# Performance work log

Measured on AMD Instinct MI355X. Metric: run time of the kernel, lower is better.

Reference implementation:

```python
import jax, jax.numpy as jnp
import numpy as np

V, E, H2, T_LEN, B, NTAG = 50257, 512, 1024, 512, 64, 7
H = H2 // 2  # per-direction hidden
START, STOP = 5, 6


def _lstm_dir(x, h0, c0, w_ih, w_hh, b_ih, b_hh, reverse=False):
    # x: [B, T, E]; returns hidden states [B, T, H]
    def step(carry, x_t):
        h, c = carry
        g = x_t @ w_ih.T + b_ih + h @ w_hh.T + b_hh  # [B, 4H]
        i, f, gg, o = jnp.split(g, 4, axis=-1)       # PyTorch gate order i,f,g,o
        c = jax.nn.sigmoid(f) * c + jax.nn.sigmoid(i) * jnp.tanh(gg)
        h = jax.nn.sigmoid(o) * jnp.tanh(c)
        return (h, c), h
    xs = jnp.swapaxes(x, 0, 1)  # [T, B, E]
    _, hs = jax.lax.scan(step, (h0, c0), xs, reverse=reverse)
    return jnp.swapaxes(hs, 0, 1)


def _viterbi(logits, transitions):
    def step(prev, logit_t):  # prev: [B, NTAG]
        v = prev[:, :, None] + transitions[None, :, :]  # [B, prev, next]
        new = logit_t + jnp.max(v, axis=1)
        bp = jnp.argmax(v, axis=1)
        return new, bp
    first = logits[:, 0]
    rest = jnp.swapaxes(logits[:, 1:], 0, 1)  # [T-1, B, NTAG]
    last, bps = jax.lax.scan(step, first, rest)
    scores = jnp.max(last, axis=-1)            # [B]
    last_tag = jnp.argmax(last, axis=-1)       # [B]

    def back(tag, bp_t):  # bp_t: [B, NTAG]
        prev = jnp.take_along_axis(bp_t, tag[:, None], axis=1)[:, 0]
        return prev, prev
    _, earlier = jax.lax.scan(back, last_tag, bps, reverse=True)  # [T-1, B], tags 0..T-2
    paths = jnp.concatenate([jnp.swapaxes(earlier, 0, 1), last_tag[:, None]], axis=1)  # [B, T]
    return scores, paths


def setup_inputs() -> dict:
    key = jax.random.key(0)
    ks = jax.random.split(key, 16)
    s = 1.0 / np.sqrt(H)
    inp = {
        "sentences": jax.random.randint(ks[0], (B, T_LEN), 0, V),
        "emb": jax.random.normal(ks[1], (V, E), jnp.float32),
        "w_ih_f": jax.random.uniform(ks[2], (4 * H, E), jnp.float32, -s, s),
        "w_hh_f": jax.random.uniform(ks[3], (4 * H, H), jnp.float32, -s, s),
        "b_ih_f": jax.random.uniform(ks[4], (4 * H,), jnp.float32, -s, s),
        "b_hh_f": jax.random.uniform(ks[5], (4 * H,), jnp.float32, -s, s),
        "w_ih_b": jax.random.uniform(ks[6], (4 * H, E), jnp.float32, -s, s),
        "w_hh_b": jax.random.uniform(ks[7], (4 * H, H), jnp.float32, -s, s),
        "b_ih_b": jax.random.uniform(ks[8], (4 * H,), jnp.float32, -s, s),
        "b_hh_b": jax.random.uniform(ks[9], (4 * H,), jnp.float32, -s, s),
        "w_out": jax.random.normal(ks[10], (NTAG, H2), jnp.float32) * 0.02,
        "b_out": jnp.zeros((NTAG,), jnp.float32),
        "h0": jax.random.normal(ks[12], (2, B, H), jnp.float32),
        "c0": jax.random.normal(ks[13], (2, B, H), jnp.float32),
    }
    trans = jax.random.normal(ks[14], (NTAG, NTAG), jnp.float32)
    trans = trans.at[START, :].set(-100.0).at[:, STOP].set(-100.0)
    inp["transitions"] = trans
    return inp


def reference(sentences, emb, w_ih_f, w_hh_f, b_ih_f, b_hh_f,
              w_ih_b, w_hh_b, b_ih_b, b_hh_b, w_out, b_out, h0, c0, transitions):
    x = emb[sentences]  # [B, T, E]
    out_f = _lstm_dir(x, h0[0], c0[0], w_ih_f, w_hh_f, b_ih_f, b_hh_f, reverse=False)
    out_b = _lstm_dir(x, h0[1], c0[1], w_ih_b, w_hh_b, b_ih_b, b_hh_b, reverse=True)
    lstm_out = jnp.concatenate([out_f, out_b], axis=-1)  # [B, T, 2H]
    logits = lstm_out @ w_out.T + b_out                  # [B, T, NTAG]
    scores, paths = _viterbi(logits, transitions)
    return scores, paths
```

## Files before the change

kernel.cpp:

```cpp
#include <hip/hip_runtime.h>
#include <cstdint>
#include <cstddef>

#define NTAG 7

typedef unsigned int u32;
typedef unsigned long long u64;
using bf16x8 = __attribute__((ext_vector_type(8))) short;
using f32x4  = __attribute__((ext_vector_type(4))) float;

#define MFMA(A,B,C) __builtin_amdgcn_mfma_f32_16x16x32_bf16((A),(B),(C),0,0,0)

union abf { u64 q[2]; ushort e[8]; bf16x8 v; };

__device__ __forceinline__ u32 rtn_bf16(float f) {
    u32 b = __float_as_uint(f);
    return (b + 0x7fffu + ((b >> 16) & 1u)) >> 16;
}

__global__ __launch_bounds__(256) void prep_w_kernel(
    const float* __restrict__ wif, const float* __restrict__ whf,
    const float* __restrict__ wib, const float* __restrict__ whb,
    ushort* __restrict__ planes)
{
    int f = blockIdx.x * 256 + threadIdx.x;
    int mat = f >> 17;
    int i8 = (f & 0x1FFFF) << 3;
    const float* src = (mat == 0) ? wif : (mat == 1) ? whf : (mat == 2) ? wib : whb;
    float4 v0 = *(const float4*)(src + i8);
    float4 v1 = *(const float4*)(src + i8 + 4);
    ushort o[8];
    const float* pv = (const float*)&v0;
#pragma unroll
    for (int j = 0; j < 4; ++j) o[j] = (ushort)rtn_bf16(pv[j]);
    pv = (const float*)&v1;
#pragma unroll
    for (int j = 0; j < 4; ++j) o[4 + j] = (ushort)rtn_bf16(pv[j]);
    ushort* dst = planes + ((size_t)mat << 20) + i8;
    *(ushort4*)dst = make_ushort4(o[0], o[1], o[2], o[3]);
    *(ushort4*)(dst + 4) = make_ushort4(o[4], o[5], o[6], o[7]);
}

__global__ __launch_bounds__(256) void prep_x_kernel(
    const int* __restrict__ sent, const float* __restrict__ emb,
    ushort* __restrict__ xb)
{
    long f = (long)blockIdx.x * 256 + threadIdx.x;
    long e8 = f << 3;
    int bt = (int)(e8 >> 9);
    int e  = (int)(e8 & 511);
    int tok = sent[bt];
    const float* src = emb + (size_t)tok * 512 + e;
    float4 v0 = *(const float4*)(src);
    float4 v1 = *(const float4*)(src + 4);
    ushort o[8];
    const float* pv = (const float*)&v0;
#pragma unroll
    for (int j = 0; j < 4; ++j) o[j] = (ushort)rtn_bf16(pv[j]);
    pv = (const float*)&v1;
#pragma unroll
    for (int j = 0; j < 4; ++j) o[4 + j] = (ushort)rtn_bf16(pv[j]);
    ushort* dst = xb + e8;
    *(ushort4*)dst = make_ushort4(o[0], o[1], o[2], o[3]);
    *(ushort4*)(dst + 4) = make_ushort4(o[4], o[5], o[6], o[7]);
}

__global__ __launch_bounds__(256, 1) void lstm_mfma_kernel(
    const int* __restrict__ sent, const float* __restrict__ emb,
    const ushort* __restrict__ planes, const ushort* __restrict__ xb,
    const float* __restrict__ bif, const float* __restrict__ bhf,
    const float* __restrict__ bib, const float* __restrict__ bhb,
    const float* __restrict__ wout,
    const float* __restrict__ h0, const float* __restrict__ c0,
    ushort* __restrict__ hglob,
    float* __restrict__ logits,
    int* __restrict__ flags)
{
    __shared__ __align__(16) ushort hstage[16 * 512];
    __shared__ float sums_s[4 * 16 * 33];
    __shared__ float hv_s[16 * 33];
    __shared__ float bias_s[4 * 32];
    __shared__ float wout_s[7 * 33];
    __shared__ float lbuf[8 * 112];

    const int tid = threadIdx.x;
    const int w   = tid >> 6;
    const int L   = tid & 63;
    const int ln  = L & 15;
    const int lk  = L >> 4;
    const int g   = blockIdx.x & 7;
    const int slot= blockIdx.x >> 3;
    const int d   = g & 1;
    const int bq  = g >> 1;
    const int B0  = bq << 4;
    const int u0  = slot << 5;

    const ushort* wip = planes + ((size_t)(d ? 2 : 0) << 20);
    const ushort* whp = planes + ((size_t)(d ? 3 : 1) << 20);

    bf16x8 Bh[2][16];
#pragma unroll
    for (int h = 0; h < 2; ++h) {
        const size_t row = (size_t)(w * 512 + u0 + h * 16 + ln);
#pragma unroll
        for (int kb = 0; kb < 16; ++kb)
            Bh[h][kb] = *(const bf16x8*)(whp + row * 512 + kb * 32 + lk * 8);
    }
    if (tid < 128) {
        int gg = tid >> 5, uu = tid & 31;
        int grow = gg * 512 + u0 + uu;
        bias_s[tid] = d ? (bib[grow] + bhb[grow]) : (bif[grow] + bhf[grow]);
    }
    if (tid < 224) {
        int tg = tid >> 5, uu = tid & 31;
        wout_s[tg * 33 + uu] = wout[(size_t)tg * 1024 + d * 512 + u0 + uu];
    }
    const int cb = tid >> 4, uh = tid & 15;
    float cst[2];
    {
        const float* cr = c0 + ((size_t)(d * 64) + B0 + cb) * 512 + u0 + uh * 2;
        cst[0] = cr[0]; cst[1] = cr[1];
    }
    __syncthreads();

    const int gb = B0 + ln;
    f32x4 xacc0, xacc1;

    auto x_phase = [&](int tnext) {
        f32x4 a0a = {0,0,0,0}, a0b = {0,0,0,0}, a1a = {0,0,0,0}, a1b = {0,0,0,0};
        const size_t row0 = (size_t)(w * 512 + u0 + ln);
        const size_t row1 = row0 + 16;
#pragma unroll
        for (int kb = 0; kb < 16; ++kb) {
            bf16x8 A;
            if (xb) {
                A = *(const bf16x8*)(xb + ((size_t)gb * 512 + tnext) * 512 + kb * 32 + lk * 8);
            } else {
                int tok = sent[gb * 512 + tnext];
                const float* xr = emb + (size_t)tok * 512 + kb * 32 + lk * 8;
                float4 f0 = *(const float4*)(xr);
                float4 f1 = *(const float4*)(xr + 4);
                abf t;
                const float* pv = (const float*)&f0;
#pragma unroll
                for (int j = 0; j < 4; ++j) t.e[j] = (ushort)rtn_bf16(pv[j]);
                pv = (const float*)&f1;
#pragma unroll
                for (int j = 0; j < 4; ++j) t.e[4 + j] = (ushort)rtn_bf16(pv[j]);
                A = t.v;
            }
            bf16x8 Bx0 = *(const bf16x8*)(wip + row0 * 512 + kb * 32 + lk * 8);
            bf16x8 Bx1 = *(const bf16x8*)(wip + row1 * 512 + kb * 32 + lk * 8);
            if (kb & 1) { a0b = MFMA(A, Bx0, a0b); a1b = MFMA(A, Bx1, a1b); }
            else        { a0a = MFMA(A, Bx0, a0a); a1a = MFMA(A, Bx1, a1a); }
        }
        xacc0 = a0a + a0b;
        xacc1 = a1a + a1b;
    };

    x_phase(d ? 511 : 0);

    const char* hsb = (const char*)hstage;
    const int hx = (ln & 7) << 4;

    for (int s = 0; s < 512; ++s) {
        const int t = d ? (511 - s) : s;

        if (s > 0 && w == 0) {
            const int* fp = flags + (g << 4) + (L & 15);
            while (true) {
                int v = __hip_atomic_load(fp, __ATOMIC_RELAXED, __HIP_MEMORY_SCOPE_AGENT);
                if (__all(v >= s)) break;
                __builtin_amdgcn_s_sleep(1);
            }
        }
        __syncthreads();

        f32x4 f0a = xacc0, f0b = {0,0,0,0}, f1a = xacc1, f1b = {0,0,0,0};
        if (s == 0) {
            const float* hr = h0 + ((size_t)(d * 64) + gb) * 512;
#pragma unroll
            for (int kb = 0; kb < 16; ++kb) {
                float4 q0 = *(const float4*)(hr + kb * 32 + lk * 8);
                float4 q1 = *(const float4*)(hr + kb * 32 + lk * 8 + 4);
                abf A;
                const float* pv = (const float*)&q0;
#pragma unroll
                for (int j = 0; j < 4; ++j) A.e[j] = (ushort)rtn_bf16(pv[j]);
                pv = (const float*)&q1;
#pragma unroll
                for (int j = 0; j < 4; ++j) A.e[4 + j] = (ushort)rtn_bf16(pv[j]);
                if (kb & 1) { f0b = MFMA(A.v, Bh[0][kb], f0b); f1b = MFMA(A.v, Bh[1][kb], f1b); }
                else        { f0a = MFMA(A.v, Bh[0][kb], f0a); f1a = MFMA(A.v, Bh[1][kb], f1a); }
            }
        } else {
            {
                const u64* hq = (const u64*)(hglob + ((size_t)((s & 1) * 2 + d) * 64 + B0) * 512);
                const int r = tid & 15, cq = tid >> 4;
                u64 tmp[8];
#pragma unroll
                for (int i = 0; i < 8; ++i)
                    tmp[i] = __hip_atomic_load(hq + r * 128 + cq * 8 + i,
                                               __ATOMIC_RELAXED, __HIP_MEMORY_SCOPE_AGENT);
                char* hd = (char*)hstage + r * 1024;
                const int rsw = (r & 7) << 4, c64 = cq * 64;
#pragma unroll
                for (int i = 0; i < 8; ++i)
                    *(u64*)(hd + ((c64 + (i >> 1) * 16) ^ rsw) + (i & 1) * 8) = tmp[i];
            }
            __syncthreads();
            abf A[16];
#pragma unroll
            for (int kb = 0; kb < 16; ++kb)
                A[kb].v = *(const bf16x8*)(hsb + ln * 1024 + ((kb * 64 + lk * 16) ^ hx));
#pragma unroll
            for (int kb = 0; kb < 16; ++kb) {
                if (kb & 1) { f0b = MFMA(A[kb].v, Bh[0][kb], f0b); f1b = MFMA(A[kb].v, Bh[1][kb], f1b); }
                else        { f0a = MFMA(A[kb].v, Bh[0][kb], f0a); f1a = MFMA(A[kb].v, Bh[1][kb], f1a); }
            }
        }
        f32x4 g0 = f0a + f0b, g1 = f1a + f1b;

#pragma unroll
        for (int r = 0; r < 4; ++r) {
            int b = lk * 4 + r;
            sums_s[w * 528 + b * 33 + ln]      = g0[r];
            sums_s[w * 528 + b * 33 + 16 + ln] = g1[r];
        }
        __syncthreads();

        {
            u32 pk = 0;
#pragma unroll
            for (int e = 0; e < 2; ++e) {
                int u = uh * 2 + e;
                float si = sums_s[0 * 528 + cb * 33 + u] + bias_s[u];
                float sf = sums_s[1 * 528 + cb * 33 + u] + bias_s[32 + u];
                float sg = sums_s[2 * 528 + cb * 33 + u] + bias_s[64 + u];
                float so = sums_s[3 * 528 + cb * 33 + u] + bias_s[96 + u];
                float ig = 1.f / (1.f + expf(-si));
                float fg = 1.f / (1.f + expf(-sf));
                float gv = tanhf(sg);
                float og = 1.f / (1.f + expf(-so));
                float cn = fg * cst[e] + ig * gv;
                cst[e] = cn;
                float hh = og * tanhf(cn);
                hv_s[cb * 33 + u] = hh;
                pk |= rtn_bf16(hh) << (16 * e);
            }
            u32* dst = (u32*)(hglob + ((size_t)(((s + 1) & 1) * 2 + d) * 64 + B0 + cb) * 512 + u0 + uh * 2);
            __hip_atomic_store(dst, pk, __ATOMIC_RELAXED, __HIP_MEMORY_SCOPE_AGENT);
        }
        __syncthreads();

        __builtin_amdgcn_s_waitcnt(0);
        __syncthreads();
        if (tid == 0)
            __hip_atomic_store(flags + (g << 4) + slot, s + 1,
                               __ATOMIC_RELAXED, __HIP_MEMORY_SCOPE_AGENT);

        if (s < 511) x_phase(d ? (510 - s) : (s + 1));

        if (tid >= 144) {
            int q = tid - 144, tg = q >> 4, b = q & 15;
            float a = 0.f;
#pragma unroll
            for (int u = 0; u < 32; ++u)
                a = fmaf(hv_s[b * 33 + u], wout_s[tg * 33 + u], a);
            lbuf[(s & 7) * 112 + q] = a;
            if ((s & 7) == 7) {
#pragma unroll
                for (int k = 0; k < 8; ++k) {
                    int sk = s - 7 + k;
                    int tk = d ? (511 - sk) : sk;
                    atomicAdd(&logits[((size_t)tk * 64 + B0 + b) * NTAG + tg],
                              lbuf[k * 112 + q]);
                }
            }
        }
    }
}

__global__ __launch_bounds__(256) void viterbi_kernel(
    const float* __restrict__ logits, const float* __restrict__ bout,
    const float* __restrict__ trans,
    unsigned char* __restrict__ bp,
    float* __restrict__ out)
{
    __shared__ float Ls[4][512][7];
    const int tid = threadIdx.x;
    const int b0 = blockIdx.x << 2;

    for (int idx = tid; idx < 4 * 512 * 7; idx += 256) {
        int bl = idx / 3584;
        int rem = idx - bl * 3584;
        int t = rem / 7;
        int tg = rem - t * 7;
        Ls[bl][t][tg] = logits[((size_t)t * 64 + b0 + bl) * 7 + tg] + bout[tg];
    }
    __syncthreads();

    const int w = tid >> 6;
    const int lane = tid & 63;
    const int b = b0 + w;
    const int k = lane;

    float tr[7];
#pragma unroll
    for (int j = 0; j < 7; ++j) tr[j] = (k < 7) ? trans[j * 7 + k] : -1e30f;
    float prev = (k < 7) ? Ls[w][0][k] : -1e30f;
    unsigned char* bpb = bp + (size_t)b * 512 * 8;

    for (int t = 1; t < 512; ++t) {
        float best = __shfl(prev, 0, 64) + tr[0];
        int bj = 0;
#pragma unroll
        for (int j = 1; j < 7; ++j) {
            float v = __shfl(prev, j, 64) + tr[j];
            if (v > best) { best = v; bj = j; }
        }
        float lv = (k < 7) ? Ls[w][t][k] : 0.f;
        if (k < 7) bpb[t * 8 + k] = (unsigned char)bj;
        prev = lv + best;
    }

    float pv[7];
#pragma unroll
    for (int j = 0; j < 7; ++j) pv[j] = __shfl(prev, j, 64);
    float best = pv[0]; int bj = 0;
#pragma unroll
    for (int j = 1; j < 7; ++j) if (pv[j] > best) { best = pv[j]; bj = j; }
    if (lane == 0) {
        out[b] = best;
        out[64 + (size_t)b * 512 + 511] = (float)bj;
    }

    int cur = bj;
    for (int tc = 448; tc >= 0; tc -= 64) {
        int t = tc + lane;
        u64 row = *(const u64*)(bpb + (size_t)t * 8);
        for (int i = 63; i >= 0; --i) {
            int t2 = tc + i;
            if (t2 < 1) break;
            u64 r = __shfl(row, i, 64);
            cur = (int)((r >> (cur * 8)) & 0xFF);
            if (lane == 0) out[64 + (size_t)b * 512 + (t2 - 1)] = (float)cur;
        }
    }
}

extern "C" void kernel_launch(void* const* d_in, const int* in_sizes, int n_in,
                              void* d_out, int out_size, void* d_ws, size_t ws_size,
                              hipStream_t stream)
{
    (void)in_sizes; (void)n_in; (void)out_size;
    const int*   sent = (const int*)d_in[0];
    const float* emb  = (const float*)d_in[1];
    const float* wif  = (const float*)d_in[2];
    const float* whf  = (const float*)d_in[3];
    const float* bif  = (const float*)d_in[4];
    const float* bhf  = (const float*)d_in[5];
    const float* wib  = (const float*)d_in[6];
    const float* whb  = (const float*)d_in[7];
    const float* bib  = (const float*)d_in[8];
    const float* bhb  = (const float*)d_in[9];
    const float* wout = (const float*)d_in[10];
    const float* bout = (const float*)d_in[11];
    const float* h0   = (const float*)d_in[12];
    const float* c0   = (const float*)d_in[13];
    const float* trans= (const float*)d_in[14];
    float* out = (float*)d_out;

    char* p = (char*)d_ws;
    float*  logits = (float*)p;            p += 917504;
    int*    flags  = (int*)p;              p += 8192;
    ushort* hglob  = (ushort*)p;           p += 2 * 2 * 64 * 512 * 2;
    unsigned char* bp = (unsigned char*)p; p += 262144;
    ushort* planes = (ushort*)p;           p += 4 * 1048576 * 2;
    size_t base_need = (size_t)(p - (char*)d_ws);
    ushort* xb = nullptr;
    if (ws_size >= base_need + (size_t)64 * 512 * 512 * 2) xb = (ushort*)p;

    hipMemsetAsync(d_ws, 0, 917504 + 8192, stream);
    prep_w_kernel<<<2048, 256, 0, stream>>>(wif, whf, wib, whb, planes);
    if (xb) prep_x_kernel<<<8192, 256, 0, stream>>>(sent, emb, xb);
    lstm_mfma_kernel<<<128, 256, 0, stream>>>(
        sent, emb, planes, xb, bif, bhf, bib, bhb,
        wout, h0, c0, hglob, logits, flags);
    viterbi_kernel<<<16, 256, 0, stream>>>(logits, bout, trans, bp, out);
}
```

Measured before the change: 5.612 ms.

## Replace logit atomics with per-block partial buffers and reorder per-step flag publication

Each LSTM block now writes its per-step logit contributions non-temporally into a per-slot partial buffer, and the Viterbi kernel reduces the 32 partials itself, replacing batched atomicAdds. The h-state staging load moves before the MFMA branch with a coalesced layout and an explicit waitcnt. The x-phase for the next step now runs before the flag store, which delays publishing the flag. The aim is to cut atomic traffic and load latency on the serial critical path, at the cost of a large extra workspace buffer and later flag signalling, which could lengthen the cross-block dependency chain.

```diff
diff --git a/kernel.cpp b/kernel.cpp
--- a/kernel.cpp
+++ b/kernel.cpp
@@ -74,6 +74,7 @@
     const float* __restrict__ h0, const float* __restrict__ c0,
     ushort* __restrict__ hglob,
     float* __restrict__ logits,
+    float* __restrict__ partial,
     int* __restrict__ flags)
 {
     __shared__ __align__(16) ushort hstage[16 * 512];
@@ -81,7 +82,6 @@
     __shared__ float hv_s[16 * 33];
     __shared__ float bias_s[4 * 32];
     __shared__ float wout_s[7 * 33];
-    __shared__ float lbuf[8 * 112];
 
     const int tid = threadIdx.x;
     const int w   = tid >> 6;
@@ -163,15 +163,51 @@
     const char* hsb = (const char*)hstage;
     const int hx = (ln & 7) << 4;
 
+#define AL(P) __hip_atomic_load((P), __ATOMIC_RELAXED, __HIP_MEMORY_SCOPE_AGENT)
+
     for (int s = 0; s < 512; ++s) {
         const int t = d ? (511 - s) : s;
 
         if (s > 0 && w == 0) {
             const int* fp = flags + (g << 4) + (L & 15);
             while (true) {
-                int v = __hip_atomic_load(fp, __ATOMIC_RELAXED, __HIP_MEMORY_SCOPE_AGENT);
+                int v = AL(fp);
                 if (__all(v >= s)) break;
                 __builtin_amdgcn_s_sleep(1);
+            }
+        }
+        __syncthreads();
+
+        if (s > 0) {
+            const u64* hq = (const u64*)(hglob + ((size_t)((s & 1) * 2 + d) * 64 + B0) * 512);
+            u64 sv0 = AL(hq + tid * 2);          u64 sv1 = AL(hq + tid * 2 + 1);
+            u64 sv2 = AL(hq + 512 + tid * 2);    u64 sv3 = AL(hq + 512 + tid * 2 + 1);
+            u64 sv4 = AL(hq + 1024 + tid * 2);   u64 sv5 = AL(hq + 1024 + tid * 2 + 1);
+            u64 sv6 = AL(hq + 1536 + tid * 2);   u64 sv7 = AL(hq + 1536 + tid * 2 + 1);
+            __builtin_amdgcn_s_waitcnt(0);
+            __builtin_amdgcn_sched_barrier(0);
+            char* hd = (char*)hstage;
+            const int c_ = (tid & 63) * 16;
+            const int r_ = tid >> 6;
+            {
+                int rr = r_;
+                char* a = hd + rr * 1024 + (c_ ^ ((rr & 7) << 4));
+                *(u64*)a = sv0; *(u64*)(a + 8) = sv1;
+            }
+            {
+                int rr = r_ + 4;
+                char* a = hd + rr * 1024 + (c_ ^ ((rr & 7) << 4));
+                *(u64*)a = sv2; *(u64*)(a + 8) = sv3;
+            }
+            {
+                int rr = r_ + 8;
+                char* a = hd + rr * 1024 + (c_ ^ ((rr & 7) << 4));
+                *(u64*)a = sv4; *(u64*)(a + 8) = sv5;
+            }
+            {
+                int rr = r_ + 12;
+                char* a = hd + rr * 1024 + (c_ ^ ((rr & 7) << 4));
+                *(u64*)a = sv6; *(u64*)(a + 8) = sv7;
             }
         }
         __syncthreads();
@@ -194,21 +230,6 @@
                 else        { f0a = MFMA(A.v, Bh[0][kb], f0a); f1a = MFMA(A.v, Bh[1][kb], f1a); }
             }
         } else {
-            {
-                const u64* hq = (const u64*)(hglob + ((size_t)((s & 1) * 2 + d) * 64 + B0) * 512);
-                const int r = tid & 15, cq = tid >> 4;
-                u64 tmp[8];
-#pragma unroll
-                for (int i = 0; i < 8; ++i)
-                    tmp[i] = __hip_atomic_load(hq + r * 128 + cq * 8 + i,
-                                               __ATOMIC_RELAXED, __HIP_MEMORY_SCOPE_AGENT);
-                char* hd = (char*)hstage + r * 1024;
-                const int rsw = (r & 7) << 4, c64 = cq * 64;
-#pragma unroll
-                for (int i = 0; i < 8; ++i)
-                    *(u64*)(hd + ((c64 + (i >> 1) * 16) ^ rsw) + (i & 1) * 8) = tmp[i];
-            }
-            __syncthreads();
             abf A[16];
 #pragma unroll
             for (int kb = 0; kb < 16; ++kb)
@@ -253,37 +274,33 @@
         }
         __syncthreads();
 
-        __builtin_amdgcn_s_waitcnt(0);
-        __syncthreads();
-        if (tid == 0)
-            __hip_atomic_store(flags + (g << 4) + slot, s + 1,
-                               __ATOMIC_RELAXED, __HIP_MEMORY_SCOPE_AGENT);
-
-        if (s < 511) x_phase(d ? (510 - s) : (s + 1));
-
         if (tid >= 144) {
             int q = tid - 144, tg = q >> 4, b = q & 15;
             float a = 0.f;
 #pragma unroll
             for (int u = 0; u < 32; ++u)
                 a = fmaf(hv_s[b * 33 + u], wout_s[tg * 33 + u], a);
-            lbuf[(s & 7) * 112 + q] = a;
-            if ((s & 7) == 7) {
-#pragma unroll
-                for (int k = 0; k < 8; ++k) {
-                    int sk = s - 7 + k;
-                    int tk = d ? (511 - sk) : sk;
-                    atomicAdd(&logits[((size_t)tk * 64 + B0 + b) * NTAG + tg],
-                              lbuf[k * 112 + q]);
-                }
-            }
-        }
-    }
+            if (partial)
+                __builtin_nontemporal_store(a, partial +
+                    ((size_t)t * 64 + B0 + b) * 224 + (slot * 2 + d) * 7 + tg);
+            else
+                atomicAdd(&logits[((size_t)t * 64 + B0 + b) * NTAG + tg], a);
+        }
+
+        if (s < 511) x_phase(d ? (510 - s) : (s + 1));
+
+        __builtin_amdgcn_s_waitcnt(0);
+        __syncthreads();
+        if (s < 511 && tid == 0)
+            __hip_atomic_store(flags + (g << 4) + slot, s + 1,
+                               __ATOMIC_RELAXED, __HIP_MEMORY_SCOPE_AGENT);
+    }
+#undef AL
 }
 
 __global__ __launch_bounds__(256) void viterbi_kernel(
-    const float* __restrict__ logits, const float* __restrict__ bout,
-    const float* __restrict__ trans,
+    const float* __restrict__ logits, const float* __restrict__ partial,
+    const float* __restrict__ bout, const float* __restrict__ trans,
     unsigned char* __restrict__ bp,
     float* __restrict__ out)
 {
@@ -291,12 +308,30 @@
     const int tid = threadIdx.x;
     const int b0 = blockIdx.x << 2;
 
-    for (int idx = tid; idx < 4 * 512 * 7; idx += 256) {
-        int bl = idx / 3584;
-        int rem = idx - bl * 3584;
-        int t = rem / 7;
-        int tg = rem - t * 7;
-        Ls[bl][t][tg] = logits[((size_t)t * 64 + b0 + bl) * 7 + tg] + bout[tg];
+    if (partial) {
+        for (int idx2 = tid; idx2 < 2048; idx2 += 256) {
+            int bl = idx2 >> 9, t = idx2 & 511;
+            const float* pp = partial + ((size_t)t * 64 + b0 + bl) * 224;
+            float a0=0,a1=0,a2=0,a3=0,a4=0,a5=0,a6=0;
+#pragma unroll 8
+            for (int c = 0; c < 32; ++c) {
+                const float* q = pp + c * 7;
+                a0 += q[0]; a1 += q[1]; a2 += q[2]; a3 += q[3];
+                a4 += q[4]; a5 += q[5]; a6 += q[6];
+            }
+            Ls[bl][t][0] = a0 + bout[0]; Ls[bl][t][1] = a1 + bout[1];
+            Ls[bl][t][2] = a2 + bout[2]; Ls[bl][t][3] = a3 + bout[3];
+            Ls[bl][t][4] = a4 + bout[4]; Ls[bl][t][5] = a5 + bout[5];
+            Ls[bl][t][6] = a6 + bout[6];
+        }
+    } else {
+        for (int idx = tid; idx < 4 * 512 * 7; idx += 256) {
+            int bl = idx / 3584;
+            int rem = idx - bl * 3584;
+            int t = rem / 7;
+            int tg = rem - t * 7;
+            Ls[bl][t][tg] = logits[((size_t)t * 64 + b0 + bl) * 7 + tg] + bout[tg];
+        }
     }
     __syncthreads();
 
@@ -379,13 +414,18 @@
     ushort* planes = (ushort*)p;           p += 4 * 1048576 * 2;
     size_t base_need = (size_t)(p - (char*)d_ws);
     ushort* xb = nullptr;
-    if (ws_size >= base_need + (size_t)64 * 512 * 512 * 2) xb = (ushort*)p;
+    float*  partial = nullptr;
+    if (ws_size >= base_need + (size_t)64 * 512 * 512 * 2) {
+        xb = (ushort*)p;  p += (size_t)64 * 512 * 512 * 2;
+        if (ws_size >= (size_t)(p - (char*)d_ws) + (size_t)512 * 64 * 224 * 4)
+            partial = (float*)p;
+    }
 
     hipMemsetAsync(d_ws, 0, 917504 + 8192, stream);
     prep_w_kernel<<<2048, 256, 0, stream>>>(wif, whf, wib, whb, planes);
     if (xb) prep_x_kernel<<<8192, 256, 0, stream>>>(sent, emb, xb);
     lstm_mfma_kernel<<<128, 256, 0, stream>>>(
         sent, emb, planes, xb, bif, bhf, bib, bhb,
-        wout, h0, c0, hglob, logits, flags);
-    viterbi_kernel<<<16, 256, 0, stream>>>(logits, bout, trans, bp, out);
-}
+        wout, h0, c0, hglob, logits, partial, flags);
+    viterbi_kernel<<<16, 256, 0, stream>>>(logits, partial, bout, trans, bp, out);
+}
```

After: 5.316 ms. 5.3% less time.
